# Kernel optimization log

Hardware: AMD Instinct MI355X
Metric: run time of the kernel (lower is better)

The kernel has to match this reference:

```python
import jax, jax.numpy as jnp
import numpy as np

INPUT_DIM = 512
QUERY_DIM = 512
NUM_HEAD = 8
HEAD_DIM = INPUT_DIM // NUM_HEAD
SQRT_INPUT_DIM = INPUT_DIM ** 0.5
ELU_CLIP = 15.0  # elu_clip: elu followed by clamp to [-15, 15] (keeps exp finite)


def elu_clip(x):
    return jnp.clip(jax.nn.elu(x), -ELU_CLIP, ELU_CLIP)


def setup_inputs() -> dict:
    key = jax.random.key(0)
    k1, k2, k3, k4, k5, k6, k7 = jax.random.split(key, 7)
    B, S, Q = 8, 4096, 32
    inputs = jax.random.normal(k1, (B, S, INPUT_DIM), dtype=jnp.float32)
    queries = jax.random.normal(k2, (B, Q, QUERY_DIM), dtype=jnp.float32)
    masks = (jax.random.uniform(k3, (B, S)) > 0.1).astype(jnp.float32)
    # torch Linear params: weight [out, in], bias [out]
    lim_kv = 1.0 / np.sqrt(INPUT_DIM)
    Wkv = jax.random.uniform(k4, (2 * INPUT_DIM, INPUT_DIM), minval=-lim_kv, maxval=lim_kv, dtype=jnp.float32)
    bkv = jax.random.uniform(k5, (2 * INPUT_DIM,), minval=-lim_kv, maxval=lim_kv, dtype=jnp.float32)
    lim_q = 1.0 / np.sqrt(QUERY_DIM)
    Wq = jax.random.uniform(k6, (INPUT_DIM, QUERY_DIM), minval=-lim_q, maxval=lim_q, dtype=jnp.float32)
    bq = jax.random.uniform(k7, (INPUT_DIM,), minval=-lim_q, maxval=lim_q, dtype=jnp.float32)
    return {"inputs": inputs, "queries": queries, "masks": masks,
            "Wkv": Wkv, "bkv": bkv, "Wq": Wq, "bq": bq}


def reference(inputs, queries, masks, Wkv, bkv, Wq, bq):
    B, S, _ = inputs.shape
    Q = queries.shape[1]
    # k, v projections: [B,S,2I] -> [B,S,2,H,D]; index 0 along dim 2 is k, 1 is v
    kv = (inputs @ Wkv.T + bkv).reshape(B, S, 2, NUM_HEAD, HEAD_DIM)
    k, v = kv[:, :, 0], kv[:, :, 1]          # [B,S,H,D]
    q = (queries @ Wq.T + bq).reshape(B, Q, NUM_HEAD, HEAD_DIM)  # [B,Q,H,D]
    # scores: broadcast dot-product per head -> [B,Q,S,H]
    u = jnp.einsum('bqhd,bshd->bqsh', q, k)
    exp_u = jnp.exp(elu_clip(u / SQRT_INPUT_DIM))
    exp_u = exp_u * masks[:, None, :, None]
    attention = exp_u / jnp.sum(exp_u, axis=2, keepdims=True)
    # weighted sum over sequence -> [B,Q,H,D] -> [B,Q,I]
    attend = jnp.einsum('bqsh,bshd->bqhd', attention, v).reshape(B, Q, INPUT_DIM)
    return attend
```

## Files before the change

### kernel.cpp

```cpp
#include <hip/hip_runtime.h>
#include <hip/hip_bf16.h>


typedef float f32x4 __attribute__((ext_vector_type(4)));
typedef short s16x8 __attribute__((ext_vector_type(8)));

__device__ __forceinline__ unsigned short f2bf(float f) {
  union { __hip_bfloat16 h; unsigned short u; } cv;
  cv.h = __float2bfloat16(f);
  return cv.u;
}
__device__ __forceinline__ float bf2f(unsigned short u) {
  union { unsigned short u; __hip_bfloat16 h; } cv;
  cv.u = u;
  return __bfloat162float(cv.h);
}
__device__ __forceinline__ float tofl(float v) { return v; }
__device__ __forceinline__ float tofl(__hip_bfloat16 v) { return __bfloat162float(v); }

__device__ __forceinline__ f32x4 mfma16(s16x8 a, s16x8 b, f32x4 c) {
  return __builtin_amdgcn_mfma_f32_16x16x32_bf16(a, b, c, 0, 0, 0);
}

__device__ __forceinline__ int detect_fp32(const unsigned short* __restrict__ in16) {
  unsigned short v = in16[2 * (threadIdx.x & 63)];
  int e = (v >> 7) & 0xFF;
  unsigned long long m = __ballot(e >= 100 && e <= 130);
  return __popcll(m) < 48 ? 1 : 0;
}

__device__ __forceinline__ void gload_lds16(const void* g, void* s) {
  __builtin_amdgcn_global_load_lds(
      (const __attribute__((address_space(1))) unsigned int*)(g),
      (__attribute__((address_space(3))) unsigned int*)(s), 16, 0, 0);
}

__device__ __forceinline__ unsigned short* stg(unsigned short* buf, int r, int u) {
  return buf + r * 64 + ((u ^ (r & 7)) << 3);
}
__device__ __forceinline__ const unsigned short* stgc(const unsigned short* buf, int r, int u) {
  return buf + r * 64 + ((u ^ (r & 7)) << 3);
}
__device__ __forceinline__ int sw_idx(int r, int c) {
  return r * 128 + ((((c >> 3) ^ (r & 7)) << 3) | (c & 7));
}

template <typename T>
__device__ __forceinline__ s16x8 load_frag8(const T* p);
template <>
__device__ __forceinline__ s16x8 load_frag8<float>(const float* p) {
  const float4* q = reinterpret_cast<const float4*>(p);
  float4 a = q[0], b = q[1];
  union { unsigned short u[8]; s16x8 w; } t;
  t.u[0] = f2bf(a.x); t.u[1] = f2bf(a.y); t.u[2] = f2bf(a.z); t.u[3] = f2bf(a.w);
  t.u[4] = f2bf(b.x); t.u[5] = f2bf(b.y); t.u[6] = f2bf(b.z); t.u[7] = f2bf(b.w);
  return t.w;
}
template <>
__device__ __forceinline__ s16x8 load_frag8<__hip_bfloat16>(const __hip_bfloat16* p) {
  return *reinterpret_cast<const s16x8*>(p);
}

template <typename T> struct RegChunk;
template <> struct RegChunk<float> {
  float4 v[4];
  __device__ __forceinline__ void load(const float* p) {
    const float4* q = reinterpret_cast<const float4*>(p);
    v[0] = q[0]; v[1] = q[1]; v[2] = q[2]; v[3] = q[3];
  }
  __device__ __forceinline__ void store(unsigned short* d) {
    union { unsigned short u[16]; s16x8 w[2]; } t;
    const float* f = reinterpret_cast<const float*>(v);
#pragma unroll
    for (int i = 0; i < 16; ++i) t.u[i] = f2bf(f[i]);
    reinterpret_cast<s16x8*>(d)[0] = t.w[0];
    reinterpret_cast<s16x8*>(d)[1] = t.w[1];
  }
  __device__ __forceinline__ void store2(unsigned short* d0, unsigned short* d1) {
    union { unsigned short u[16]; s16x8 w[2]; } t;
    const float* f = reinterpret_cast<const float*>(v);
#pragma unroll
    for (int i = 0; i < 16; ++i) t.u[i] = f2bf(f[i]);
    *reinterpret_cast<s16x8*>(d0) = t.w[0];
    *reinterpret_cast<s16x8*>(d1) = t.w[1];
  }
};
template <> struct RegChunk<__hip_bfloat16> {
  s16x8 v[2];
  __device__ __forceinline__ void load(const __hip_bfloat16* p) {
    const s16x8* q = reinterpret_cast<const s16x8*>(p);
    v[0] = q[0]; v[1] = q[1];
  }
  __device__ __forceinline__ void store(unsigned short* d) {
    reinterpret_cast<s16x8*>(d)[0] = v[0];
    reinterpret_cast<s16x8*>(d)[1] = v[1];
  }
  __device__ __forceinline__ void store2(unsigned short* d0, unsigned short* d1) {
    *reinterpret_cast<s16x8*>(d0) = v[0];
    *reinterpret_cast<s16x8*>(d1) = v[1];
  }
};


#define CINP 0
#define CQ   16777216
#define CWKV 16908288
#define CWQ  17432576
#define CBKV 17694720
#define CBQ  17695744
#define CTOT 17696256

__global__ __launch_bounds__(256) void k_conv(const void* inputs, const void* queries,
                                              const void* Wkv, const void* Wq,
                                              const void* bkv, const void* bq,
                                              unsigned short* __restrict__ dst) {
  const int fp32 = detect_fp32((const unsigned short*)inputs);
  size_t i8 = (size_t)blockIdx.x * 256 + threadIdx.x;
  const size_t total8 = CTOT / 8;
  for (; i8 < total8; i8 += (size_t)2048 * 256) {
    size_t e = i8 * 8;
    const void* src;
    size_t off;
    if (e < CQ) { src = inputs; off = e - CINP; }
    else if (e < CWKV) { src = queries; off = e - CQ; }
    else if (e < CWQ) { src = Wkv; off = e - CWKV; }
    else if (e < CBKV) { src = Wq; off = e - CWQ; }
    else if (e < CBQ) { src = bkv; off = e - CBKV; }
    else { src = bq; off = e - CBQ; }
    s16x8 v;
    if (fp32)
      v = load_frag8<float>((const float*)src + off);
    else
      v = load_frag8<__hip_bfloat16>((const __hip_bfloat16*)src + off);
    *reinterpret_cast<s16x8*>(dst + e) = v;
  }
}

__global__ __launch_bounds__(256) void k_gemm2(const unsigned short* __restrict__ c,
                                               unsigned short* __restrict__ kv,
                                               unsigned short* __restrict__ qws) {
  __shared__ unsigned short Ab[128 * 64];
  __shared__ unsigned short Bb[128 * 64];

  const int bid = blockIdx.x;
  const int t = (bid & 7) * 257 + (bid >> 3);
  const unsigned short *A, *W, *bias;
  unsigned short* dst;
  int dstride, Mt, Nt;
  if (t < 2048) {
    A = c + CINP; W = c + CWKV; bias = c + CBKV;
    dst = kv; dstride = 1024; Mt = t >> 3; Nt = t & 7;
  } else {
    const int tq = t - 2048;
    A = c + CQ; W = c + CWQ; bias = c + CBQ;
    dst = qws; dstride = 512; Mt = tq >> 2; Nt = tq & 3;
  }

  const int tid = threadIdx.x;
  const int w = tid >> 6, l = tid & 63;
  const int quad = l >> 4, l16 = l & 15;
  const int wr = (w >> 1) * 64, wc = (w & 1) * 64;

  const int lrow = l >> 3;
  const int gsw = (l & 7) ^ lrow;

  const f32x4 zero4 = {0.f, 0.f, 0.f, 0.f};
  f32x4 acc[4][4];
#pragma unroll
  for (int i = 0; i < 4; ++i)
#pragma unroll
    for (int j = 0; j < 4; ++j) acc[i][j] = zero4;

  const size_t arow0 = (size_t)(Mt * 128) * 512;
  const size_t brow0 = (size_t)(Nt * 128) * 512;

#pragma unroll
  for (int k0 = 0; k0 < 512; k0 += 64) {
    __syncthreads();
#pragma unroll
    for (int k = 0; k < 4; ++k) {
      const int row = w * 32 + k * 8 + lrow;
      const int srcc = k0 + gsw * 8;
      gload_lds16(A + arow0 + (size_t)row * 512 + srcc, Ab + (w * 32 + k * 8) * 64);
      gload_lds16(W + brow0 + (size_t)row * 512 + srcc, Bb + (w * 32 + k * 8) * 64);
    }
    __syncthreads();
#pragma unroll
    for (int kk2 = 0; kk2 < 2; ++kk2) {
      s16x8 af[4], bfr[4];
#pragma unroll
      for (int i = 0; i < 4; ++i)
        af[i] = *reinterpret_cast<const s16x8*>(stgc(Ab, wr + i * 16 + l16, kk2 * 4 + quad));
#pragma unroll
      for (int j = 0; j < 4; ++j)
        bfr[j] = *reinterpret_cast<const s16x8*>(stgc(Bb, wc + j * 16 + l16, kk2 * 4 + quad));
#pragma unroll
      for (int i = 0; i < 4; ++i)
#pragma unroll
        for (int j = 0; j < 4; ++j) acc[i][j] = mfma16(af[i], bfr[j], acc[i][j]);
    }
  }

#pragma unroll
  for (int j = 0; j < 4; ++j) {
    float bb = bf2f(bias[Nt * 128 + wc + j * 16 + l16]);
#pragma unroll
    for (int i = 0; i < 4; ++i)
#pragma unroll
      for (int rg = 0; rg < 4; ++rg) {
        int row = Mt * 128 + wr + i * 16 + quad * 4 + rg;
        int col = Nt * 128 + wc + j * 16 + l16;
        dst[(size_t)row * dstride + col] = f2bf(acc[i][j][rg] + bb);
      }
  }
}

template <typename T>
__device__ __forceinline__ void attn_body(const unsigned short* __restrict__ kv,
                                          const unsigned short* __restrict__ qws,
                                          const T* __restrict__ masks,
                                          float* __restrict__ num_part,
                                          float* __restrict__ den_part,
                                          unsigned short* kvb, unsigned short* vtb,
                                          unsigned short* Pb, float* denL) {
  const int stile = blockIdx.x, b = blockIdx.y;
  const int s0 = stile * 128;
  const int tid = threadIdx.x;
  const int w = tid >> 6, l = tid & 63;
  const int quad = l >> 4, l16 = l & 15;
  const int hh = w >> 2, mt = (w >> 1) & 1, sh = w & 1, dh = w & 1;
  const int sr2 = tid >> 2, c0 = (tid & 3) * 32;
  const f32x4 zero4 = {0.f, 0.f, 0.f, 0.f};
  const float scale = 0.044194173824159216f;
  const int bstile = b * 32 + stile;

  for (int hpi = 0; hpi < 4; ++hpi) {
    const unsigned short* kr =
        kv + ((size_t)(b * 4096 + s0 + sr2)) * 1024 + hpi * 128 + c0;
#pragma unroll
    for (int j = 0; j < 4; ++j)
      *reinterpret_cast<s16x8*>(&kvb[sw_idx(sr2, c0 + j * 8)]) =
          *reinterpret_cast<const s16x8*>(kr + j * 8);
    const unsigned short* vr = kr + 512;
#pragma unroll
    for (int j = 0; j < 4; ++j) {
      union { s16x8 wv; unsigned short u[8]; } tv;
      tv.wv = *reinterpret_cast<const s16x8*>(vr + j * 8);
#pragma unroll
      for (int e = 0; e < 8; ++e) vtb[sw_idx(c0 + j * 8 + e, sr2)] = tv.u[e];
    }
    __syncthreads();

    {
      f32x4 ua[4];
#pragma unroll
      for (int j = 0; j < 4; ++j) ua[j] = zero4;
#pragma unroll
      for (int kk = 0; kk < 2; ++kk) {
        s16x8 aq = *reinterpret_cast<const s16x8*>(
            &qws[((size_t)(b * 32 + mt * 16 + l16)) * 512 + hpi * 128 + hh * 64 + kk * 32 +
                 quad * 8]);
#pragma unroll
        for (int j = 0; j < 4; ++j) {
          s16x8 bk = *reinterpret_cast<const s16x8*>(
              &kvb[sw_idx(sh * 64 + j * 16 + l16, hh * 64 + kk * 32 + quad * 8)]);
          ua[j] = mfma16(aq, bk, ua[j]);
        }
      }
      float dsum[4] = {0.f, 0.f, 0.f, 0.f};
#pragma unroll
      for (int j = 0; j < 4; ++j) {
        int scol = sh * 64 + j * 16 + l16;
        float mask = tofl(masks[(size_t)b * 4096 + s0 + scol]);
#pragma unroll
        for (int rg = 0; rg < 4; ++rg) {
          int qrow = mt * 16 + quad * 4 + rg;
          float uv = ua[j][rg] * scale;
          float e = uv > 0.f ? uv : (__expf(uv) - 1.f);
          e = fminf(e, 15.f);
          float p = __expf(e) * mask;
          unsigned short pu = f2bf(p);
          Pb[sw_idx(hh * 32 + qrow, scol)] = pu;
          dsum[rg] += bf2f(pu);
        }
      }
#pragma unroll
      for (int rg = 0; rg < 4; ++rg) {
        float s = dsum[rg];
        s += __shfl_xor(s, 1);
        s += __shfl_xor(s, 2);
        s += __shfl_xor(s, 4);
        s += __shfl_xor(s, 8);
        if (l16 == 0) denL[sh * 64 + hh * 32 + mt * 16 + quad * 4 + rg] = s;
      }
    }
    __syncthreads();

    if (tid < 64) {
      int qrow = tid & 31, hd = tid >> 5;
      den_part[((size_t)bstile * 32 + qrow) * 8 + hpi * 2 + hd] =
          denL[hd * 32 + qrow] + denL[64 + hd * 32 + qrow];
    }

    {
      f32x4 na0 = zero4, na1 = zero4;
#pragma unroll
      for (int kk = 0; kk < 4; ++kk) {
        s16x8 ap = *reinterpret_cast<const s16x8*>(
            &Pb[sw_idx(hh * 32 + mt * 16 + l16, kk * 32 + quad * 8)]);
        s16x8 bv0 = *reinterpret_cast<const s16x8*>(
            &vtb[sw_idx(hh * 64 + dh * 32 + l16, kk * 32 + quad * 8)]);
        s16x8 bv1 = *reinterpret_cast<const s16x8*>(
            &vtb[sw_idx(hh * 64 + dh * 32 + 16 + l16, kk * 32 + quad * 8)]);
        na0 = mfma16(ap, bv0, na0);
        na1 = mfma16(ap, bv1, na1);
      }
#pragma unroll
      for (int rg = 0; rg < 4; ++rg) {
        int qrow = mt * 16 + quad * 4 + rg;
        size_t base = ((size_t)bstile * 32 + qrow) * 512 + (hpi * 2 + hh) * 64 + dh * 32;
        num_part[base + l16] = na0[rg];
        num_part[base + 16 + l16] = na1[rg];
      }
    }
    __syncthreads();
  }
}

__global__ __launch_bounds__(512) void k_attn(const unsigned short* __restrict__ kv,
                                              const unsigned short* __restrict__ qws,
                                              const void* masks, float* __restrict__ num_part,
                                              float* __restrict__ den_part,
                                              const unsigned short* __restrict__ det) {
  __shared__ unsigned short kvb[128 * 128];
  __shared__ unsigned short vtb[128 * 128];
  __shared__ unsigned short Pb[64 * 128];
  __shared__ float denL[128];
  if (detect_fp32(det))
    attn_body<float>(kv, qws, (const float*)masks, num_part, den_part, kvb, vtb, Pb, denL);
  else
    attn_body<__hip_bfloat16>(kv, qws, (const __hip_bfloat16*)masks, num_part, den_part,
                              kvb, vtb, Pb, denL);
}

__global__ __launch_bounds__(256) void k_final(const float* __restrict__ num_part,
                                               const float* __restrict__ den_part, void* out,
                                               const unsigned short* __restrict__ det) {
  int i = blockIdx.x * 256 + threadIdx.x;
  int b = i >> 14, qhd = i & 16383;
  int q = (i >> 9) & 31, h = (i >> 6) & 7;
  float sn = 0.f, sd = 0.f;
#pragma unroll 4
  for (int st = 0; st < 32; ++st) {
    sn += num_part[(((size_t)(b * 32 + st)) << 14) + qhd];
    sd += den_part[((size_t)(b * 32 + st) * 32 + q) * 8 + h];
  }
  float v = sn / sd;
  if (detect_fp32(det))
    ((float*)out)[i] = v;
  else
    ((__hip_bfloat16*)out)[i] = __float2bfloat16(v);
}

template <typename T>
__device__ __forceinline__ void qproj_body_fb(const T* __restrict__ queries,
                                              const T* __restrict__ Wq,
                                              const T* __restrict__ bq,
                                              unsigned short* __restrict__ qws,
                                              unsigned short* Abuf, unsigned short* Bbuf) {
  const int Mt = blockIdx.x, Nt = blockIdx.y;
  const int tid = threadIdx.x;
  const int w = tid >> 6, l = tid & 63;
  const int quad = l >> 4, l16 = l & 15;
  const int wr = (w >> 1) * 64, wc = (w & 1) * 64;
  const int r_st = tid >> 1;
  const int kk_st = (tid & 1) * 16;
  const T* Asrc = queries + ((size_t)(Mt * 128 + r_st)) * 512 + kk_st;
  const T* Bsrc = Wq + ((size_t)(Nt * 128 + r_st)) * 512 + kk_st;

  const f32x4 zero4 = {0.f, 0.f, 0.f, 0.f};
  f32x4 acc[4][4];
#pragma unroll
  for (int i = 0; i < 4; ++i)
#pragma unroll
    for (int j = 0; j < 4; ++j) acc[i][j] = zero4;

  RegChunk<T> ra, rb;
  ra.load(Asrc);
  rb.load(Bsrc);
  for (int k0 = 0; k0 < 512; k0 += 32) {
    __syncthreads();
    ra.store(&Abuf[r_st * 32 + kk_st]);
    rb.store(&Bbuf[r_st * 32 + kk_st]);
    if (k0 + 32 < 512) {
      ra.load(Asrc + k0 + 32);
      rb.load(Bsrc + k0 + 32);
    }
    __syncthreads();
    s16x8 af[4], bfr[4];
#pragma unroll
    for (int i = 0; i < 4; ++i)
      af[i] = *reinterpret_cast<const s16x8*>(&Abuf[(wr + i * 16 + l16) * 32 + quad * 8]);
#pragma unroll
    for (int j = 0; j < 4; ++j)
      bfr[j] = *reinterpret_cast<const s16x8*>(&Bbuf[(wc + j * 16 + l16) * 32 + quad * 8]);
#pragma unroll
    for (int i = 0; i < 4; ++i)
#pragma unroll
      for (int j = 0; j < 4; ++j) acc[i][j] = mfma16(af[i], bfr[j], acc[i][j]);
  }
#pragma unroll
  for (int j = 0; j < 4; ++j) {
    float bb = tofl(bq[Nt * 128 + wc + j * 16 + l16]);
#pragma unroll
    for (int i = 0; i < 4; ++i)
#pragma unroll
      for (int rg = 0; rg < 4; ++rg) {
        int row = Mt * 128 + wr + i * 16 + quad * 4 + rg;
        int col = Nt * 128 + wc + j * 16 + l16;
        qws[(size_t)row * 512 + col] = f2bf(acc[i][j][rg] + bb);
      }
  }
}

__global__ __launch_bounds__(256) void k_qproj_fb(const void* queries, const void* Wq,
                                                  const void* bq, unsigned short* qws,
                                                  const unsigned short* __restrict__ det) {
  __shared__ unsigned short Abuf[128 * 32];
  __shared__ unsigned short Bbuf[128 * 32];
  if (detect_fp32(det))
    qproj_body_fb<float>((const float*)queries, (const float*)Wq, (const float*)bq, qws,
                         Abuf, Bbuf);
  else
    qproj_body_fb<__hip_bfloat16>((const __hip_bfloat16*)queries,
                                  (const __hip_bfloat16*)Wq, (const __hip_bfloat16*)bq, qws,
                                  Abuf, Bbuf);
}

template <typename T>
__device__ __forceinline__ void fused_body_fb(
    const T* __restrict__ inputs, const T* __restrict__ masks, const T* __restrict__ Wkv,
    const T* __restrict__ bkv, const unsigned short* __restrict__ qws,
    float* __restrict__ num, float* __restrict__ den, unsigned short* Abuf,
    unsigned short* Bbuf, unsigned short* kvbuf, unsigned short* vbuf,
    unsigned short* Pbuf) {
  const int stile = blockIdx.x;
  const int b = blockIdx.y;
  const int hp = blockIdx.z;
  const int s0 = stile * 128;
  const int tid = threadIdx.x;
  const int w = tid >> 6;
  const int l = tid & 63;
  const int quad = l >> 4;
  const int l16 = l & 15;
  const int which = w >> 2;
  const int wr = ((w >> 1) & 1) * 64;
  const int wc = (w & 1) * 64;

  const f32x4 zero4 = {0.f, 0.f, 0.f, 0.f};
  f32x4 acc[4][4];
#pragma unroll
  for (int i = 0; i < 4; ++i)
#pragma unroll
    for (int j = 0; j < 4; ++j) acc[i][j] = zero4;

  const int sr = tid >> 2;
  const int sc = tid & 3;
  const T* Asrc = inputs + ((size_t)(b * 4096 + s0 + sr)) * 512 + sc * 16;
  const T* BKs = Wkv + ((size_t)(hp * 128 + sr)) * 512 + sc * 16;
  const T* BVs = Wkv + ((size_t)(512 + hp * 128 + sr)) * 512 + sc * 16;
  unsigned short* ad0 = stg(Abuf, sr, sc * 2);
  unsigned short* ad1 = stg(Abuf, sr, sc * 2 + 1);
  unsigned short* bk0 = stg(Bbuf, sr, sc * 2);
  unsigned short* bk1 = stg(Bbuf, sr, sc * 2 + 1);
  unsigned short* bv0 = stg(Bbuf, 128 + sr, sc * 2);
  unsigned short* bv1 = stg(Bbuf, 128 + sr, sc * 2 + 1);

  RegChunk<T> ra0, ra1, rbk, rbv;
  ra0.load(Asrc);
  ra1.load(Asrc + 64);
  rbk.load(BKs);
  rbv.load(BVs);

#pragma unroll
  for (int it2 = 0; it2 < 4; ++it2) {
#pragma unroll
    for (int ph = 0; ph < 2; ++ph) {
      const int it = it2 * 2 + ph;
      RegChunk<T>& ra = ph ? ra1 : ra0;
      __syncthreads();
      ra.store2(ad0, ad1);
      rbk.store2(bk0, bk1);
      rbv.store2(bv0, bv1);
      if (it < 6) ra.load(Asrc + (it + 2) * 64);
      if (it < 7) {
        rbk.load(BKs + (it + 1) * 64);
        rbv.load(BVs + (it + 1) * 64);
      }
      __syncthreads();
#pragma unroll
      for (int kk2 = 0; kk2 < 2; ++kk2) {
        s16x8 af[4], bfr[4];
#pragma unroll
        for (int i = 0; i < 4; ++i)
          af[i] = *reinterpret_cast<const s16x8*>(stgc(Abuf, wr + i * 16 + l16, kk2 * 4 + quad));
#pragma unroll
        for (int j = 0; j < 4; ++j)
          bfr[j] = *reinterpret_cast<const s16x8*>(
              stgc(Bbuf, which * 128 + wc + j * 16 + l16, kk2 * 4 + quad));
#pragma unroll
        for (int i = 0; i < 4; ++i)
#pragma unroll
          for (int j = 0; j < 4; ++j) acc[i][j] = mfma16(af[i], bfr[j], acc[i][j]);
      }
    }
  }

#pragma unroll
  for (int j = 0; j < 4; ++j) {
    float bb = tofl(bkv[which * 512 + hp * 128 + wc + j * 16 + l16]);
#pragma unroll
    for (int i = 0; i < 4; ++i)
#pragma unroll
      for (int rg = 0; rg < 4; ++rg) {
        int sl = wr + i * 16 + quad * 4 + rg;
        int c = wc + j * 16 + l16;
        unsigned short bv = f2bf(acc[i][j][rg] + bb);
        if (which == 0)
          kvbuf[sw_idx(sl, c)] = bv;
        else
          vbuf[sw_idx(c, sl)] = bv;
      }
  }
  __syncthreads();

  const int hh = w >> 2, mt = (w >> 1) & 1, sh = w & 1;
  {
    f32x4 ua[4];
#pragma unroll
    for (int j = 0; j < 4; ++j) ua[j] = zero4;
#pragma unroll
    for (int kk = 0; kk < 2; ++kk) {
      s16x8 aq = *reinterpret_cast<const s16x8*>(
          qws + ((size_t)(b * 32 + mt * 16 + l16)) * 512 + hp * 128 + hh * 64 + kk * 32 +
          quad * 8);
#pragma unroll
      for (int j = 0; j < 4; ++j) {
        s16x8 bk = *reinterpret_cast<const s16x8*>(
            &kvbuf[sw_idx(sh * 64 + j * 16 + l16, hh * 64 + kk * 32 + quad * 8)]);
        ua[j] = mfma16(aq, bk, ua[j]);
      }
    }
    const float scale = 0.044194173824159216f;
    float dsum[4] = {0.f, 0.f, 0.f, 0.f};
#pragma unroll
    for (int j = 0; j < 4; ++j) {
      int scol = sh * 64 + j * 16 + l16;
      float mask = tofl(masks[(size_t)b * 4096 + s0 + scol]);
#pragma unroll
      for (int rg = 0; rg < 4; ++rg) {
        int qrow = mt * 16 + quad * 4 + rg;
        float uv = ua[j][rg] * scale;
        float e = uv > 0.f ? uv : (__expf(uv) - 1.f);
        e = fminf(e, 15.f);
        float p = __expf(e) * mask;
        unsigned short pu = f2bf(p);
        Pbuf[sw_idx(hh * 32 + qrow, scol)] = pu;
        dsum[rg] += bf2f(pu);
      }
    }
#pragma unroll
    for (int rg = 0; rg < 4; ++rg) {
      float s = dsum[rg];
      s += __shfl_xor(s, 1);
      s += __shfl_xor(s, 2);
      s += __shfl_xor(s, 4);
      s += __shfl_xor(s, 8);
      if (l16 == 0) {
        int qrow = mt * 16 + quad * 4 + rg;
        atomicAdd(&den[((size_t)(b * 32 + qrow)) * 8 + hp * 2 + hh], s);
      }
    }
  }
  __syncthreads();

  {
    const int dh = w & 1;
    f32x4 na[2];
    na[0] = zero4;
    na[1] = zero4;
#pragma unroll
    for (int kk = 0; kk < 4; ++kk) {
      s16x8 ap = *reinterpret_cast<const s16x8*>(
          &Pbuf[sw_idx(hh * 32 + mt * 16 + l16, kk * 32 + quad * 8)]);
#pragma unroll
      for (int jj = 0; jj < 2; ++jj) {
        int j = dh * 2 + jj;
        s16x8 bv = *reinterpret_cast<const s16x8*>(
            &vbuf[sw_idx(hh * 64 + j * 16 + l16, kk * 32 + quad * 8)]);
        na[jj] = mfma16(ap, bv, na[jj]);
      }
    }
    const int h = hp * 2 + hh;
#pragma unroll
    for (int jj = 0; jj < 2; ++jj) {
      int d = (dh * 2 + jj) * 16 + l16;
#pragma unroll
      for (int rg = 0; rg < 4; ++rg) {
        int qrow = mt * 16 + quad * 4 + rg;
        atomicAdd(&num[(((size_t)(b * 32 + qrow)) * 8 + h) * 64 + d], na[jj][rg]);
      }
    }
  }
}

__global__ __launch_bounds__(512, 2) void k_fused_fb(const void* inputs, const void* masks,
                                                     const void* Wkv, const void* bkv,
                                                     const unsigned short* __restrict__ qws,
                                                     float* __restrict__ num,
                                                     float* __restrict__ den) {
  __shared__ unsigned short Abuf[128 * 64];
  __shared__ unsigned short Bbuf[256 * 64];
  __shared__ unsigned short kvbuf[128 * 128];
  __shared__ unsigned short vbuf[128 * 128];
  __shared__ unsigned short Pbuf[64 * 128];
  if (detect_fp32((const unsigned short*)inputs))
    fused_body_fb<float>((const float*)inputs, (const float*)masks, (const float*)Wkv,
                         (const float*)bkv, qws, num, den, Abuf, Bbuf, kvbuf, vbuf, Pbuf);
  else
    fused_body_fb<__hip_bfloat16>((const __hip_bfloat16*)inputs,
                                  (const __hip_bfloat16*)masks, (const __hip_bfloat16*)Wkv,
                                  (const __hip_bfloat16*)bkv, qws, num, den, Abuf, Bbuf,
                                  kvbuf, vbuf, Pbuf);
}

__global__ __launch_bounds__(256) void k_div_fb(const float* __restrict__ num,
                                                const float* __restrict__ den, void* out,
                                                const unsigned short* __restrict__ det) {
  int i = blockIdx.x * 256 + threadIdx.x;
  float v = num[i] / den[i >> 6];
  if (detect_fp32(det))
    ((float*)out)[i] = v;
  else
    ((__hip_bfloat16*)out)[i] = __float2bfloat16(v);
}

extern "C" void kernel_launch(void* const* d_in, const int* in_sizes, int n_in,
                              void* d_out, int out_size, void* d_ws, size_t ws_size,
                              hipStream_t stream) {
  char* ws = (char*)d_ws;
  if (ws_size >= 119802880) {
    unsigned short* conv = (unsigned short*)ws;
    unsigned short* kv = (unsigned short*)(ws + 35392512);
    unsigned short* qws = (unsigned short*)(ws + 102501376);
    float* num_part = (float*)(ws + 102763520);
    float* den_part = (float*)(ws + 119540736);

    k_conv<<<2048, 256, 0, stream>>>(d_in[0], d_in[1], d_in[3], d_in[5], d_in[4], d_in[6],
                                     conv);
    k_gemm2<<<2056, 256, 0, stream>>>(conv, kv, qws);
    k_attn<<<dim3(32, 8), 512, 0, stream>>>(kv, qws, d_in[2], num_part, den_part,
                                            (const unsigned short*)d_in[0]);
    k_final<<<512, 256, 0, stream>>>(num_part, den_part, d_out,
                                     (const unsigned short*)d_in[0]);
  } else if (ws_size >= 802816) {
    float* den = (float*)(ws + 1024);
    float* num = (float*)(ws + 16384);
    unsigned short* qws = (unsigned short*)(ws + 540672);

    hipMemsetAsync(d_ws, 0, 540672, stream);
    dim3 gq(2, 4);
    k_qproj_fb<<<gq, 256, 0, stream>>>(d_in[1], d_in[5], d_in[6], qws,
                                       (const unsigned short*)d_in[0]);
    dim3 g2(32, 8, 4);
    k_fused_fb<<<g2, 512, 0, stream>>>(d_in[0], d_in[2], d_in[3], d_in[4], qws, num, den);
    k_div_fb<<<512, 256, 0, stream>>>(num, den, d_out, (const unsigned short*)d_in[0]);
  }
}
```

Measured before the change: 182.4 us.

## Prefetch next head-pair K/V into registers and pack V transpose stores

In the attention kernel, K/V for the next head pair are loaded into registers before the barrier so the global loads overlap the current MFMA work. The V transpose now writes two sequence rows per 32-bit LDS store instead of scalar 16-bit stores. The conversion kernel also gets a dedicated unrolled path for the large inputs tensor plus a separate 72-block tail for the smaller tensors, so the big copy no longer branches per element. This raises register pressure in the attention kernel in exchange for latency hiding.

```diff
diff --git a/kernel.cpp b/kernel.cpp
--- a/kernel.cpp
+++ b/kernel.cpp
@@ -115,24 +115,37 @@
                                               const void* bkv, const void* bq,
                                               unsigned short* __restrict__ dst) {
   const int fp32 = detect_fp32((const unsigned short*)inputs);
-  size_t i8 = (size_t)blockIdx.x * 256 + threadIdx.x;
-  const size_t total8 = CTOT / 8;
-  for (; i8 < total8; i8 += (size_t)2048 * 256) {
-    size_t e = i8 * 8;
-    const void* src;
-    size_t off;
-    if (e < CQ) { src = inputs; off = e - CINP; }
-    else if (e < CWKV) { src = queries; off = e - CQ; }
-    else if (e < CWQ) { src = Wkv; off = e - CWKV; }
-    else if (e < CBKV) { src = Wq; off = e - CWQ; }
-    else if (e < CBQ) { src = bkv; off = e - CBKV; }
-    else { src = bq; off = e - CBQ; }
-    s16x8 v;
-    if (fp32)
-      v = load_frag8<float>((const float*)src + off);
-    else
-      v = load_frag8<__hip_bfloat16>((const __hip_bfloat16*)src + off);
-    *reinterpret_cast<s16x8*>(dst + e) = v;
+  const int bid = blockIdx.x, tid = threadIdx.x;
+  if (bid < 2048) {
+    size_t u = (size_t)bid * 1024 + tid;
+#pragma unroll
+    for (int k = 0; k < 4; ++k, u += 256) {
+      size_t e = u * 8;
+      s16x8 v;
+      if (fp32)
+        v = load_frag8<float>((const float*)inputs + e);
+      else
+        v = load_frag8<__hip_bfloat16>((const __hip_bfloat16*)inputs + e);
+      *reinterpret_cast<s16x8*>(dst + e) = v;
+    }
+  } else {
+    size_t i8 = (size_t)(bid - 2048) * 256 + tid;
+    for (; i8 < 114880; i8 += (size_t)72 * 256) {
+      size_t e = CQ + i8 * 8;
+      const void* src;
+      size_t off;
+      if (e < CWKV) { src = queries; off = e - CQ; }
+      else if (e < CWQ) { src = Wkv; off = e - CWKV; }
+      else if (e < CBKV) { src = Wq; off = e - CWQ; }
+      else if (e < CBQ) { src = bkv; off = e - CBKV; }
+      else { src = bq; off = e - CBQ; }
+      s16x8 v;
+      if (fp32)
+        v = load_frag8<float>((const float*)src + off);
+      else
+        v = load_frag8<__hip_bfloat16>((const __hip_bfloat16*)src + off);
+      *reinterpret_cast<s16x8*>(dst + e) = v;
+    }
   }
 }
 
@@ -230,25 +243,50 @@
   const int quad = l >> 4, l16 = l & 15;
   const int hh = w >> 2, mt = (w >> 1) & 1, sh = w & 1, dh = w & 1;
   const int sr2 = tid >> 2, c0 = (tid & 3) * 32;
+  const int rp2 = (tid >> 3) * 2;
+  const int cb = (tid & 7) * 16;
   const f32x4 zero4 = {0.f, 0.f, 0.f, 0.f};
   const float scale = 0.044194173824159216f;
   const int bstile = b * 32 + stile;
 
+  const unsigned short* kbase = kv + ((size_t)(b * 4096 + s0 + sr2)) * 1024;
+  const unsigned short* vbase0 = kv + ((size_t)(b * 4096 + s0 + rp2)) * 1024 + 512;
+  const unsigned short* vbase1 = vbase0 + 1024;
+
+  s16x8 kp0, kp1, kp2, kp3, va0, va1, vb0, vb1;
+  auto loadKV = [&](int hpi) {
+    const unsigned short* kr = kbase + hpi * 128 + c0;
+    kp0 = *reinterpret_cast<const s16x8*>(kr);
+    kp1 = *reinterpret_cast<const s16x8*>(kr + 8);
+    kp2 = *reinterpret_cast<const s16x8*>(kr + 16);
+    kp3 = *reinterpret_cast<const s16x8*>(kr + 24);
+    const unsigned short* v0 = vbase0 + hpi * 128 + cb;
+    const unsigned short* v1 = vbase1 + hpi * 128 + cb;
+    va0 = *reinterpret_cast<const s16x8*>(v0);
+    va1 = *reinterpret_cast<const s16x8*>(v0 + 8);
+    vb0 = *reinterpret_cast<const s16x8*>(v1);
+    vb1 = *reinterpret_cast<const s16x8*>(v1 + 8);
+  };
+  loadKV(0);
+
+#pragma unroll
   for (int hpi = 0; hpi < 4; ++hpi) {
-    const unsigned short* kr =
-        kv + ((size_t)(b * 4096 + s0 + sr2)) * 1024 + hpi * 128 + c0;
-#pragma unroll
-    for (int j = 0; j < 4; ++j)
-      *reinterpret_cast<s16x8*>(&kvb[sw_idx(sr2, c0 + j * 8)]) =
-          *reinterpret_cast<const s16x8*>(kr + j * 8);
-    const unsigned short* vr = kr + 512;
-#pragma unroll
-    for (int j = 0; j < 4; ++j) {
-      union { s16x8 wv; unsigned short u[8]; } tv;
-      tv.wv = *reinterpret_cast<const s16x8*>(vr + j * 8);
-#pragma unroll
-      for (int e = 0; e < 8; ++e) vtb[sw_idx(c0 + j * 8 + e, sr2)] = tv.u[e];
-    }
+    *reinterpret_cast<s16x8*>(&kvb[sw_idx(sr2, c0)]) = kp0;
+    *reinterpret_cast<s16x8*>(&kvb[sw_idx(sr2, c0 + 8)]) = kp1;
+    *reinterpret_cast<s16x8*>(&kvb[sw_idx(sr2, c0 + 16)]) = kp2;
+    *reinterpret_cast<s16x8*>(&kvb[sw_idx(sr2, c0 + 24)]) = kp3;
+    {
+      union { s16x8 w; unsigned short u[8]; } a0, a1, b0, b1;
+      a0.w = va0; a1.w = va1; b0.w = vb0; b1.w = vb1;
+#pragma unroll
+      for (int e = 0; e < 8; ++e) {
+        unsigned int p0 = (unsigned int)a0.u[e] | ((unsigned int)b0.u[e] << 16);
+        *reinterpret_cast<unsigned int*>(&vtb[sw_idx(cb + e, rp2)]) = p0;
+        unsigned int p1 = (unsigned int)a1.u[e] | ((unsigned int)b1.u[e] << 16);
+        *reinterpret_cast<unsigned int*>(&vtb[sw_idx(cb + 8 + e, rp2)]) = p1;
+      }
+    }
+    if (hpi < 3) loadKV(hpi + 1);
     __syncthreads();
 
     {
@@ -656,7 +694,7 @@
     float* num_part = (float*)(ws + 102763520);
     float* den_part = (float*)(ws + 119540736);
 
-    k_conv<<<2048, 256, 0, stream>>>(d_in[0], d_in[1], d_in[3], d_in[5], d_in[4], d_in[6],
+    k_conv<<<2120, 256, 0, stream>>>(d_in[0], d_in[1], d_in[3], d_in[5], d_in[4], d_in[6],
                                      conv);
     k_gemm2<<<2056, 256, 0, stream>>>(conv, kv, qws);
     k_attn<<<dim3(32, 8), 512, 0, stream>>>(kv, qws, d_in[2], num_part, den_part,
```

Result: no change. 184.1 us (+0.9%).
